# Performance work log

Hardware: AMD Instinct MI355X
Metric: run time of the kernel (lower is better)

Reference implementation:

```python
import jax, jax.numpy as jnp
from jax import lax
import numpy as np

D_MODEL = 1024
N_HEADS = 16
D_STATE = D_MODEL // N_HEADS  # 64
EPS = 1e-6


def setup_inputs() -> dict:
    key = jax.random.key(0)
    ks = jax.random.split(key, 8)
    B, S = 4, 4096
    s = 1.0 / np.sqrt(D_MODEL)
    return {
        "x": jax.random.normal(ks[0], (B, S, D_MODEL), dtype=jnp.float32),
        "state": jnp.zeros((B, N_HEADS, D_STATE), dtype=jnp.float32),
        "norm_w": jnp.ones((D_MODEL,), dtype=jnp.float32),
        "Wp": jax.random.normal(ks[1], (D_MODEL, 3 * N_HEADS * D_STATE), dtype=jnp.float32) * s,
        "bp": jax.random.normal(ks[2], (3 * N_HEADS * D_STATE,), dtype=jnp.float32) * 0.01,
        "Wg": jax.random.normal(ks[3], (D_MODEL, D_MODEL), dtype=jnp.float32) * s,
        "bg": jax.random.normal(ks[4], (D_MODEL,), dtype=jnp.float32) * 0.01,
        "Wo": jax.random.normal(ks[5], (D_MODEL, D_MODEL), dtype=jnp.float32) * s,
        "bo": jax.random.normal(ks[6], (D_MODEL,), dtype=jnp.float32) * 0.01,
    }


def reference(x, state, norm_w, Wp, bp, Wg, bg, Wo, bo):
    B, S, D = x.shape
    # RMSNorm
    rms = jnp.sqrt(jnp.mean(x * x, axis=-1, keepdims=True) + EPS)
    xn = norm_w * x / rms
    # input-dependent gate and SSM parameters (all per-timestep, vectorized)
    gate = jax.nn.sigmoid(xn @ Wg + bg)                        # (B,S,D)
    p = (xn @ Wp + bp).reshape(B, S, N_HEADS, 3, D_STATE)
    delta = jax.nn.sigmoid(p[..., 0, :])                       # (B,S,H,Ds)
    Bt = p[..., 1, :]
    Ct = p[..., 2, :]
    # sequential recurrence h_{t+1} = delta_t * h_t + B_t via lax.scan over time
    def step(h, db):
        d, b = db
        h = d * h + b
        return h, h
    dT = jnp.moveaxis(delta, 1, 0)  # (S,B,H,Ds)
    bT = jnp.moveaxis(Bt, 1, 0)
    new_state, hs = lax.scan(step, state, (dT, bT))
    hs = jnp.moveaxis(hs, 0, 1)     # (B,S,H,Ds)
    ssm = (Ct * hs).reshape(B, S, D)
    mixed = gate * ssm + (1.0 - gate) * xn
    y = mixed @ Wo + bo + x         # out_proj + residual (dropout=0)
    return y, new_state
```

## Files before the change

### kernel.cpp

```cpp
#include <hip/hip_runtime.h>
#include <hip/hip_bf16.h>
#include <cstdint>
#include <cstddef>

#define D_MODEL 1024
#define N_HEADS 16
#define D_STATE 64
#define SEQ 4096
#define BATCH 4
#define M_TOK (BATCH * SEQ)
#define N1 4096
#define CLEN 128
#define NCH (SEQ / CLEN)
#define NCHAN (BATCH * D_MODEL)

typedef __attribute__((ext_vector_type(8))) short bf16x8;
typedef __attribute__((ext_vector_type(4))) float f32x4;

__device__ __forceinline__ float sigmoidf_(float x) {
    return 1.0f / (1.0f + __expf(-x));
}

__device__ __forceinline__ void async_load16(const void* g, void* l) {
    __builtin_amdgcn_global_load_lds(
        (__attribute__((address_space(1))) void*)(g),
        (__attribute__((address_space(3))) void*)(l), 16, 0, 0);
}

__global__ __launch_bounds__(256) void transpose_cvt(
    const float* __restrict__ src, __hip_bfloat16* __restrict__ dst,
    int K, int N)
{
    __shared__ float tile[32][33];
    int n0 = blockIdx.x * 32, k0 = blockIdx.y * 32;
    int tx = threadIdx.x, ty = threadIdx.y;
#pragma unroll
    for (int j = 0; j < 32; j += 8)
        tile[ty + j][tx] = src[(size_t)(k0 + ty + j) * N + n0 + tx];
    __syncthreads();
#pragma unroll
    for (int j = 0; j < 32; j += 8)
        dst[(size_t)(n0 + ty + j) * K + k0 + tx] = __float2bfloat16(tile[tx][ty + j]);
}

__global__ __launch_bounds__(256) void rmsnorm_kernel(
    const float* __restrict__ x, const float* __restrict__ w,
    __hip_bfloat16* __restrict__ xn)
{
    int m = blockIdx.x;
    int tid = threadIdx.x;
    const float4* xr = (const float4*)(x + (size_t)m * D_MODEL);
    float4 v = xr[tid];
    float ss = v.x * v.x + v.y * v.y + v.z * v.z + v.w * v.w;
#pragma unroll
    for (int o = 32; o >= 1; o >>= 1) ss += __shfl_xor(ss, o, 64);
    __shared__ float red[4];
    int wave = tid >> 6, lane = tid & 63;
    if (lane == 0) red[wave] = ss;
    __syncthreads();
    float tot = red[0] + red[1] + red[2] + red[3];
    float scale = rsqrtf(tot * (1.0f / D_MODEL) + 1e-6f);
    const float4* wr = (const float4*)w;
    float4 wv = wr[tid];
    __hip_bfloat16 o4[4];
    o4[0] = __float2bfloat16(wv.x * v.x * scale);
    o4[1] = __float2bfloat16(wv.y * v.y * scale);
    o4[2] = __float2bfloat16(wv.z * v.z * scale);
    o4[3] = __float2bfloat16(wv.w * v.w * scale);
    *(uint64_t*)(xn + (size_t)m * D_MODEL + tid * 4) = *(uint64_t*)o4;
}


template <int MODE>
__global__ __launch_bounds__(512, 2) void gemm256(
    const __hip_bfloat16* __restrict__ A,
    const __hip_bfloat16* __restrict__ Bt,
    const float* __restrict__ bias0,
    const float* __restrict__ bias1,
    void* __restrict__ outp, int N, int K)
{
    extern __shared__ short lds[];
    const int tid = threadIdx.x;
    const int wave = tid >> 6, lane = tid & 63;
    const int fr = lane & 15, fq = lane >> 4;
    const int frx = fr & 7;
    const int wm = (wave >> 2) * 128;
    const int wn = (wave & 3) * 64;

    const int gx = gridDim.x;
    const int nwg = gx * gridDim.y;
    const int orig = blockIdx.y * gx + blockIdx.x;
    const int swz = (orig & 7) * (nwg >> 3) + (orig >> 3);
    const int m0 = (swz / gx) * 256;
    const int n0 = (swz % gx) * 256;

    const int rb = tid >> 3, p8 = tid & 7;
    const int lsl = p8 ^ (rb & 7);
    const short* Ag0 = (const short*)A + (size_t)(m0 + rb) * K + lsl * 8;
    const short* Bg0 = (const short*)Bt + (size_t)(n0 + rb) * K + lsl * 8;
    const int stL = rb * 64 + p8 * 8;

    const int NT = K >> 6;

    f32x4 acc[2][4][4];
#pragma unroll
    for (int h = 0; h < 2; ++h)
#pragma unroll
        for (int i = 0; i < 4; ++i)
#pragma unroll
            for (int j = 0; j < 4; ++j)
                acc[h][i][j] = (f32x4){0.f, 0.f, 0.f, 0.f};

    {
        short* la = lds;
        short* lb = lds + 16384;
        async_load16(Bg0 + (size_t)(0 * 64) * K, lb + stL + 0 * 4096);
        async_load16(Bg0 + (size_t)(1 * 64) * K, lb + stL + 1 * 4096);
        async_load16(Bg0 + (size_t)(2 * 64) * K, lb + stL + 2 * 4096);
        async_load16(Bg0 + (size_t)(3 * 64) * K, lb + stL + 3 * 4096);
        async_load16(Ag0 + (size_t)(0 * 64) * K, la + stL + 0 * 4096);
        async_load16(Ag0 + (size_t)(2 * 64) * K, la + stL + 2 * 4096);
        async_load16(Ag0 + (size_t)(1 * 64) * K, la + stL + 1 * 4096);
        async_load16(Ag0 + (size_t)(3 * 64) * K, la + stL + 3 * 4096);
    }
    asm volatile("s_waitcnt vmcnt(2)" ::: "memory");
    __builtin_amdgcn_s_barrier();
    __builtin_amdgcn_sched_barrier(0);

#define LDA_(base, h, i, kk) (*(const bf16x8*)&(base)[(wm + (h)*64 + (i)*16 + fr) * 64 + \
                                                      (((kk)*4 + fq) ^ frx) * 8])
#define LDB_(base, j, kk)    (*(const bf16x8*)&(base)[(wn + (j)*16 + fr) * 64 + \
                                                      (((kk)*4 + fq) ^ frx) * 8])
#define STAGE_A(c) async_load16(AgN + (size_t)((c) * 64) * K, laN + stL + (c) * 4096)
#define STAGE_B(c) async_load16(BgN + (size_t)((c) * 64) * K, lbN + stL + (c) * 4096)

    bf16x8 afA[4][2], afB[4][2], b0[2][2], b1[2][2];

    {
        const short* Ab = lds;
        const short* Bb = lds + 16384;
#pragma unroll
        for (int i = 0; i < 4; ++i) { afA[i][0] = LDA_(Ab, 0, i, 0); afA[i][1] = LDA_(Ab, 0, i, 1); }
#pragma unroll
        for (int j = 0; j < 2; ++j) { b0[j][0] = LDB_(Bb, j, 0); b0[j][1] = LDB_(Bb, j, 1); }
    }

    for (int t = 0; t < NT; ++t) {
        const short* Ab = lds + ((t & 1) ? 32768 : 0);
        const short* Bb = Ab + 16384;
        short* laN = lds + ((t & 1) ? 0 : 32768);
        short* lbN = laN + 16384;
        const short* AgN = Ag0 + (size_t)(t + 1) * 64;
        const short* BgN = Bg0 + (size_t)(t + 1) * 64;
        const bool pf = (t + 1 < NT);

        if (pf) { STAGE_B(0); STAGE_B(1); }
#pragma unroll
        for (int j = 0; j < 2; ++j) { b1[j][0] = LDB_(Bb, 2 + j, 0); b1[j][1] = LDB_(Bb, 2 + j, 1); }
        __builtin_amdgcn_s_setprio(1);
#pragma unroll
        for (int i = 0; i < 4; ++i)
#pragma unroll
            for (int j = 0; j < 2; ++j) {
                acc[0][i][j] = __builtin_amdgcn_mfma_f32_16x16x32_bf16(afA[i][0], b0[j][0], acc[0][i][j], 0, 0, 0);
                acc[0][i][j] = __builtin_amdgcn_mfma_f32_16x16x32_bf16(afA[i][1], b0[j][1], acc[0][i][j], 0, 0, 0);
            }
        __builtin_amdgcn_s_setprio(0);
        __builtin_amdgcn_sched_barrier(0);

        if (pf) { STAGE_B(2); STAGE_B(3); }
        if (pf) { asm volatile("s_waitcnt vmcnt(4)" ::: "memory"); }
        else    { asm volatile("s_waitcnt vmcnt(0)" ::: "memory"); }
        __builtin_amdgcn_s_barrier();
        __builtin_amdgcn_sched_barrier(0);
#pragma unroll
        for (int i = 0; i < 4; ++i) { afB[i][0] = LDA_(Ab, 1, i, 0); afB[i][1] = LDA_(Ab, 1, i, 1); }
        __builtin_amdgcn_s_setprio(1);
#pragma unroll
        for (int i = 0; i < 4; ++i)
#pragma unroll
            for (int j = 0; j < 2; ++j) {
                acc[0][i][2 + j] = __builtin_amdgcn_mfma_f32_16x16x32_bf16(afA[i][0], b1[j][0], acc[0][i][2 + j], 0, 0, 0);
                acc[0][i][2 + j] = __builtin_amdgcn_mfma_f32_16x16x32_bf16(afA[i][1], b1[j][1], acc[0][i][2 + j], 0, 0, 0);
            }
        __builtin_amdgcn_s_setprio(0);
        __builtin_amdgcn_sched_barrier(0);

        if (pf) { STAGE_A(0); STAGE_A(2); }
        __builtin_amdgcn_s_setprio(1);
#pragma unroll
        for (int i = 0; i < 4; ++i)
#pragma unroll
            for (int j = 0; j < 2; ++j) {
                acc[1][i][j] = __builtin_amdgcn_mfma_f32_16x16x32_bf16(afB[i][0], b0[j][0], acc[1][i][j], 0, 0, 0);
                acc[1][i][j] = __builtin_amdgcn_mfma_f32_16x16x32_bf16(afB[i][1], b0[j][1], acc[1][i][j], 0, 0, 0);
            }
        __builtin_amdgcn_s_setprio(0);
        __builtin_amdgcn_sched_barrier(0);

        if (pf) {
            STAGE_A(1); STAGE_A(3);
            asm volatile("s_waitcnt vmcnt(2)" ::: "memory");
            __builtin_amdgcn_s_barrier();
            __builtin_amdgcn_sched_barrier(0);
            const short* AbN = laN;
            const short* BbN = lbN;
#pragma unroll
            for (int i = 0; i < 4; ++i) { afA[i][0] = LDA_(AbN, 0, i, 0); afA[i][1] = LDA_(AbN, 0, i, 1); }
#pragma unroll
            for (int j = 0; j < 2; ++j) { b0[j][0] = LDB_(BbN, j, 0); b0[j][1] = LDB_(BbN, j, 1); }
        }
        __builtin_amdgcn_s_setprio(1);
#pragma unroll
        for (int i = 0; i < 4; ++i)
#pragma unroll
            for (int j = 0; j < 2; ++j) {
                acc[1][i][2 + j] = __builtin_amdgcn_mfma_f32_16x16x32_bf16(afB[i][0], b1[j][0], acc[1][i][2 + j], 0, 0, 0);
                acc[1][i][2 + j] = __builtin_amdgcn_mfma_f32_16x16x32_bf16(afB[i][1], b1[j][1], acc[1][i][2 + j], 0, 0, 0);
            }
        __builtin_amdgcn_s_setprio(0);
        __builtin_amdgcn_sched_barrier(0);
    }
#undef LDA_
#undef LDB_
#undef STAGE_A
#undef STAGE_B

    if constexpr (MODE == 0) {
        __hip_bfloat16* O = (__hip_bfloat16*)outp;
        float bv[4];
#pragma unroll
        for (int j = 0; j < 4; ++j) {
            int gcol = n0 + wn + j * 16 + fr;
            bv[j] = (gcol < D_MODEL) ? bias0[gcol] : bias1[gcol - D_MODEL];
        }
#pragma unroll
        for (int h = 0; h < 2; ++h)
#pragma unroll
            for (int i = 0; i < 4; ++i)
#pragma unroll
                for (int r = 0; r < 4; ++r) {
                    int grow = m0 + wm + h * 64 + i * 16 + fq * 4 + r;
                    __hip_bfloat16* orow = O + (size_t)grow * N + n0 + wn + fr;
#pragma unroll
                    for (int j = 0; j < 4; ++j)
                        orow[j * 16] = __float2bfloat16(acc[h][i][j][r] + bv[j]);
                }
    } else {
        float* O = (float*)outp;
#pragma unroll
        for (int h = 0; h < 2; ++h)
#pragma unroll
            for (int i = 0; i < 4; ++i)
#pragma unroll
                for (int r = 0; r < 4; ++r) {
                    int grow = m0 + wm + h * 64 + i * 16 + fq * 4 + r;
#pragma unroll
                    for (int j = 0; j < 4; ++j) {
                        int gcol = n0 + wn + j * 16 + fr;
                        O[(size_t)grow * N + gcol] =
                            acc[h][i][j][r] + bias0[gcol] + bias1[(size_t)grow * D_MODEL + gcol];
                    }
                }
    }
}

__global__ __launch_bounds__(256) void scan_part1(
    const __hip_bfloat16* __restrict__ out1,
    float* __restrict__ Abuf, float* __restrict__ Bbuf)
{
    int g = blockIdx.x * 256 + threadIdx.x;
    int chan = g & (NCHAN - 1);
    int c = g >> 12;
    int b = chan >> 10;
    int hd = chan & 1023;
    int h = hd >> 6, d = hd & 63;
    size_t tok0 = (size_t)b * SEQ + (size_t)c * CLEN;
    const __hip_bfloat16* pd = out1 + tok0 * N1 + D_MODEL + h * 192 + d;
    float a = 1.0f, hloc = 0.0f;
#pragma unroll 4
    for (int s = 0; s < CLEN; s++) {
        float dp = __bfloat162float(pd[0]);
        float bt = __bfloat162float(pd[64]);
        float sd = sigmoidf_(dp);
        a *= sd;
        hloc = sd * hloc + bt;
        pd += N1;
    }
    Abuf[c * NCHAN + chan] = a;
    Bbuf[c * NCHAN + chan] = hloc;
}

__global__ __launch_bounds__(256) void scan_comb(
    const float* __restrict__ Abuf, const float* __restrict__ Bbuf,
    const float* __restrict__ state, float* __restrict__ Pbuf,
    float* __restrict__ new_state)
{
    int chan = blockIdx.x * 256 + threadIdx.x;
    float hp = state[chan];
#pragma unroll
    for (int c = 0; c < NCH; c++) {
        Pbuf[c * NCHAN + chan] = hp;
        hp = Abuf[c * NCHAN + chan] * hp + Bbuf[c * NCHAN + chan];
    }
    new_state[chan] = hp;
}

__global__ __launch_bounds__(256) void scan_apply(
    const __hip_bfloat16* __restrict__ out1,
    const __hip_bfloat16* __restrict__ xn,
    const float* __restrict__ Pbuf,
    __hip_bfloat16* __restrict__ mixed)
{
    int g = blockIdx.x * 256 + threadIdx.x;
    int chan = g & (NCHAN - 1);
    int c = g >> 12;
    int b = chan >> 10;
    int hd = chan & 1023;
    int h = hd >> 6, d = hd & 63;
    size_t tok0 = (size_t)b * SEQ + (size_t)c * CLEN;
    const __hip_bfloat16* rbase = out1 + tok0 * N1;
    const __hip_bfloat16* xbase = xn + tok0 * D_MODEL + hd;
    __hip_bfloat16* mbase = mixed + tok0 * D_MODEL + hd;
    const int pcol = D_MODEL + h * 192 + d;
    float hh = Pbuf[c * NCHAN + chan];
#pragma unroll 4
    for (int s = 0; s < CLEN; s++) {
        const __hip_bfloat16* r = rbase + (size_t)s * N1;
        float dp = __bfloat162float(r[pcol]);
        float bt = __bfloat162float(r[pcol + 64]);
        float ct = __bfloat162float(r[pcol + 128]);
        float gp = __bfloat162float(r[hd]);
        float sd = sigmoidf_(dp);
        hh = sd * hh + bt;
        float gg = sigmoidf_(gp);
        float xv = __bfloat162float(xbase[(size_t)s * D_MODEL]);
        mbase[(size_t)s * D_MODEL] = __float2bfloat16(gg * (ct * hh) + (1.0f - gg) * xv);
    }
}

extern "C" void kernel_launch(void* const* d_in, const int* in_sizes, int n_in,
                              void* d_out, int out_size, void* d_ws, size_t ws_size,
                              hipStream_t stream) {
    const float* x      = (const float*)d_in[0];
    const float* state  = (const float*)d_in[1];
    const float* norm_w = (const float*)d_in[2];
    const float* Wp     = (const float*)d_in[3];
    const float* bp     = (const float*)d_in[4];
    const float* Wg     = (const float*)d_in[5];
    const float* bg     = (const float*)d_in[6];
    const float* Wo     = (const float*)d_in[7];
    const float* bo     = (const float*)d_in[8];
    float* out = (float*)d_out;

    __hip_bfloat16* W1T   = (__hip_bfloat16*)d_ws;
    __hip_bfloat16* WoT   = W1T + (size_t)N1 * D_MODEL;
    __hip_bfloat16* xnb   = WoT + (size_t)D_MODEL * D_MODEL;
    __hip_bfloat16* out1  = xnb + (size_t)M_TOK * D_MODEL;
    __hip_bfloat16* mixed = out1 + (size_t)M_TOK * N1;
    float* Abuf = (float*)(mixed + (size_t)M_TOK * D_MODEL);
    float* Bbuf = Abuf + (size_t)NCHAN * NCH;
    float* Pbuf = Bbuf + (size_t)NCHAN * NCH;

    static bool attr_set = false;
    if (!attr_set) {
        hipFuncSetAttribute(reinterpret_cast<const void*>(&gemm256<0>),
                            hipFuncAttributeMaxDynamicSharedMemorySize, 131072);
        hipFuncSetAttribute(reinterpret_cast<const void*>(&gemm256<1>),
                            hipFuncAttributeMaxDynamicSharedMemorySize, 131072);
        attr_set = true;
    }

    dim3 tb(32, 8);
    transpose_cvt<<<dim3(1024 / 32, 1024 / 32), tb, 0, stream>>>(Wg, W1T, 1024, 1024);
    transpose_cvt<<<dim3(3072 / 32, 1024 / 32), tb, 0, stream>>>(
        Wp, W1T + (size_t)D_MODEL * D_MODEL, 1024, 3072);
    transpose_cvt<<<dim3(1024 / 32, 1024 / 32), tb, 0, stream>>>(Wo, WoT, 1024, 1024);

    rmsnorm_kernel<<<M_TOK, 256, 0, stream>>>(x, norm_w, xnb);

    gemm256<0><<<dim3(N1 / 256, M_TOK / 256), 512, 131072, stream>>>(
        xnb, W1T, bg, bp, (void*)out1, N1, D_MODEL);

    scan_part1<<<(NCHAN * NCH) / 256, 256, 0, stream>>>(out1, Abuf, Bbuf);
    scan_comb<<<NCHAN / 256, 256, 0, stream>>>(
        Abuf, Bbuf, state, Pbuf, out + (size_t)M_TOK * D_MODEL);
    scan_apply<<<(NCHAN * NCH) / 256, 256, 0, stream>>>(out1, xnb, Pbuf, mixed);

    gemm256<1><<<dim3(D_MODEL / 256, M_TOK / 256), 512, 131072, stream>>>(
        mixed, WoT, bo, x, (void*)out, D_MODEL, D_MODEL);
}
```

Before: 391.4 us.

## Fuse prep kernels, permute Wp columns, vectorize scans and drop combine kernel

Merges the three weight transposes and RMSNorm into one launch. It permutes Wp columns so delta/B/C become contiguous 1024-wide blocks, and vectorizes the scan kernels to handle four channels per thread with bf16x4 loads. It removes the separate scan_comb kernel by having each chunk recompute its prefix state from the chunk summaries, and halves the chunk length. It also precomputes LDS fragment addresses in the GEMM. These changes cut launch count and uncoalesced scalar loads, at the cost of redundant prefix work that grows with chunk index.

```diff
diff --git a/kernel.cpp b/kernel.cpp
--- a/kernel.cpp
+++ b/kernel.cpp
@@ -10,15 +10,24 @@
 #define BATCH 4
 #define M_TOK (BATCH * SEQ)
 #define N1 4096
-#define CLEN 128
+#define CLEN 64
 #define NCH (SEQ / CLEN)
 #define NCHAN (BATCH * D_MODEL)
 
 typedef __attribute__((ext_vector_type(8))) short bf16x8;
+typedef __attribute__((ext_vector_type(4))) short bf16x4;
 typedef __attribute__((ext_vector_type(4))) float f32x4;
 
 __device__ __forceinline__ float sigmoidf_(float x) {
     return 1.0f / (1.0f + __expf(-x));
+}
+__device__ __forceinline__ float b2f(short s) {
+    union { float f; unsigned u; } v; v.u = ((unsigned)(unsigned short)s) << 16;
+    return v.f;
+}
+__device__ __forceinline__ short f2b(float f) {
+    __hip_bfloat16 h = __float2bfloat16(f);
+    return *(short*)&h;
 }
 
 __device__ __forceinline__ void async_load16(const void* g, void* l) {
@@ -27,49 +36,61 @@
         (__attribute__((address_space(3))) void*)(l), 16, 0, 0);
 }
 
-__global__ __launch_bounds__(256) void transpose_cvt(
-    const float* __restrict__ src, __hip_bfloat16* __restrict__ dst,
-    int K, int N)
+__global__ __launch_bounds__(256) void prep_kernel(
+    const float* __restrict__ Wg, const float* __restrict__ Wp,
+    const float* __restrict__ Wo,
+    const float* __restrict__ x, const float* __restrict__ norm_w,
+    __hip_bfloat16* __restrict__ W1T, __hip_bfloat16* __restrict__ WoT,
+    __hip_bfloat16* __restrict__ xn)
 {
     __shared__ float tile[32][33];
-    int n0 = blockIdx.x * 32, k0 = blockIdx.y * 32;
-    int tx = threadIdx.x, ty = threadIdx.y;
-#pragma unroll
-    for (int j = 0; j < 32; j += 8)
-        tile[ty + j][tx] = src[(size_t)(k0 + ty + j) * N + n0 + tx];
-    __syncthreads();
-#pragma unroll
-    for (int j = 0; j < 32; j += 8)
-        dst[(size_t)(n0 + ty + j) * K + k0 + tx] = __float2bfloat16(tile[tx][ty + j]);
-}
-
-__global__ __launch_bounds__(256) void rmsnorm_kernel(
-    const float* __restrict__ x, const float* __restrict__ w,
-    __hip_bfloat16* __restrict__ xn)
-{
-    int m = blockIdx.x;
-    int tid = threadIdx.x;
-    const float4* xr = (const float4*)(x + (size_t)m * D_MODEL);
-    float4 v = xr[tid];
-    float ss = v.x * v.x + v.y * v.y + v.z * v.z + v.w * v.w;
-#pragma unroll
-    for (int o = 32; o >= 1; o >>= 1) ss += __shfl_xor(ss, o, 64);
     __shared__ float red[4];
-    int wave = tid >> 6, lane = tid & 63;
-    if (lane == 0) red[wave] = ss;
-    __syncthreads();
-    float tot = red[0] + red[1] + red[2] + red[3];
-    float scale = rsqrtf(tot * (1.0f / D_MODEL) + 1e-6f);
-    const float4* wr = (const float4*)w;
-    float4 wv = wr[tid];
-    __hip_bfloat16 o4[4];
-    o4[0] = __float2bfloat16(wv.x * v.x * scale);
-    o4[1] = __float2bfloat16(wv.y * v.y * scale);
-    o4[2] = __float2bfloat16(wv.z * v.z * scale);
-    o4[3] = __float2bfloat16(wv.w * v.w * scale);
-    *(uint64_t*)(xn + (size_t)m * D_MODEL + tid * 4) = *(uint64_t*)o4;
-}
-
+    const int bid = blockIdx.x;
+    const int tid = threadIdx.x;
+
+    if (bid < 5120) {
+        const float* src; __hip_bfloat16* dst; int N, bx, by, perm;
+        if (bid < 1024)      { src = Wg; dst = W1T; N = 1024; bx = bid & 31;          by = bid >> 5;          perm = 0; }
+        else if (bid < 4096) { int l = bid - 1024; src = Wp; dst = W1T; N = 3072; bx = l % 96; by = l / 96;   perm = 1; }
+        else                 { int l = bid - 4096; src = Wo; dst = WoT; N = 1024; bx = l & 31; by = l >> 5;   perm = 0; }
+        int n0 = bx * 32, k0 = by * 32;
+        int tx = tid & 31, ty = tid >> 5;
+#pragma unroll
+        for (int j = 0; j < 32; j += 8)
+            tile[ty + j][tx] = src[(size_t)(k0 + ty + j) * N + n0 + tx];
+        __syncthreads();
+#pragma unroll
+        for (int j = 0; j < 32; j += 8) {
+            int n = n0 + ty + j;
+            int row;
+            if (perm) {
+                int ht = n >> 6;
+                row = 1024 + (ht % 3) * 1024 + (ht / 3) * 64 + (n & 63);
+            } else row = n;
+            dst[(size_t)row * D_MODEL + k0 + tx] = __float2bfloat16(tile[tx][ty + j]);
+        }
+    } else {
+        int m = bid - 5120;
+        const float4* xr = (const float4*)(x + (size_t)m * D_MODEL);
+        float4 v = xr[tid];
+        float ss = v.x * v.x + v.y * v.y + v.z * v.z + v.w * v.w;
+#pragma unroll
+        for (int o = 32; o >= 1; o >>= 1) ss += __shfl_xor(ss, o, 64);
+        int wave = tid >> 6, lane = tid & 63;
+        if (lane == 0) red[wave] = ss;
+        __syncthreads();
+        float tot = red[0] + red[1] + red[2] + red[3];
+        float scale = rsqrtf(tot * (1.0f / D_MODEL) + 1e-6f);
+        const float4* wr = (const float4*)norm_w;
+        float4 wv = wr[tid];
+        __hip_bfloat16 o4[4];
+        o4[0] = __float2bfloat16(wv.x * v.x * scale);
+        o4[1] = __float2bfloat16(wv.y * v.y * scale);
+        o4[2] = __float2bfloat16(wv.z * v.z * scale);
+        o4[3] = __float2bfloat16(wv.w * v.w * scale);
+        *(uint64_t*)(xn + (size_t)m * D_MODEL + tid * 4) = *(uint64_t*)o4;
+    }
+}
 
 template <int MODE>
 __global__ __launch_bounds__(512, 2) void gemm256(
@@ -100,6 +121,11 @@
     const short* Bg0 = (const short*)Bt + (size_t)(n0 + rb) * K + lsl * 8;
     const int stL = rb * 64 + p8 * 8;
 
+    const int laneA = (wm + fr) * 128;
+    const int laneB = (wn + fr) * 128;
+    const int F0 = (fq ^ frx) * 16;
+    const int F1 = ((4 + fq) ^ frx) * 16;
+
     const int NT = K >> 6;
 
     f32x4 acc[2][4][4];
@@ -127,22 +153,21 @@
     __builtin_amdgcn_s_barrier();
     __builtin_amdgcn_sched_barrier(0);
 
-#define LDA_(base, h, i, kk) (*(const bf16x8*)&(base)[(wm + (h)*64 + (i)*16 + fr) * 64 + \
-                                                      (((kk)*4 + fq) ^ frx) * 8])
-#define LDB_(base, j, kk)    (*(const bf16x8*)&(base)[(wn + (j)*16 + fr) * 64 + \
-                                                      (((kk)*4 + fq) ^ frx) * 8])
+#define RD(base, off) (*(const bf16x8*)((base) + (off)))
 #define STAGE_A(c) async_load16(AgN + (size_t)((c) * 64) * K, laN + stL + (c) * 4096)
 #define STAGE_B(c) async_load16(BgN + (size_t)((c) * 64) * K, lbN + stL + (c) * 4096)
 
     bf16x8 afA[4][2], afB[4][2], b0[2][2], b1[2][2];
 
     {
-        const short* Ab = lds;
-        const short* Bb = lds + 16384;
-#pragma unroll
-        for (int i = 0; i < 4; ++i) { afA[i][0] = LDA_(Ab, 0, i, 0); afA[i][1] = LDA_(Ab, 0, i, 1); }
-#pragma unroll
-        for (int j = 0; j < 2; ++j) { b0[j][0] = LDB_(Bb, j, 0); b0[j][1] = LDB_(Bb, j, 1); }
+        const char* bA0 = (const char*)lds + laneA + F0;
+        const char* bA1 = (const char*)lds + laneA + F1;
+        const char* bB0 = (const char*)(lds + 16384) + laneB + F0;
+        const char* bB1 = (const char*)(lds + 16384) + laneB + F1;
+#pragma unroll
+        for (int i = 0; i < 4; ++i) { afA[i][0] = RD(bA0, i * 2048); afA[i][1] = RD(bA1, i * 2048); }
+#pragma unroll
+        for (int j = 0; j < 2; ++j) { b0[j][0] = RD(bB0, j * 2048); b0[j][1] = RD(bB1, j * 2048); }
     }
 
     for (int t = 0; t < NT; ++t) {
@@ -153,10 +178,14 @@
         const short* AgN = Ag0 + (size_t)(t + 1) * 64;
         const short* BgN = Bg0 + (size_t)(t + 1) * 64;
         const bool pf = (t + 1 < NT);
+        const char* bA0 = (const char*)Ab + laneA + F0;
+        const char* bA1 = (const char*)Ab + laneA + F1;
+        const char* bB0 = (const char*)Bb + laneB + F0;
+        const char* bB1 = (const char*)Bb + laneB + F1;
 
         if (pf) { STAGE_B(0); STAGE_B(1); }
 #pragma unroll
-        for (int j = 0; j < 2; ++j) { b1[j][0] = LDB_(Bb, 2 + j, 0); b1[j][1] = LDB_(Bb, 2 + j, 1); }
+        for (int j = 0; j < 2; ++j) { b1[j][0] = RD(bB0, (2 + j) * 2048); b1[j][1] = RD(bB1, (2 + j) * 2048); }
         __builtin_amdgcn_s_setprio(1);
 #pragma unroll
         for (int i = 0; i < 4; ++i)
@@ -174,7 +203,7 @@
         __builtin_amdgcn_s_barrier();
         __builtin_amdgcn_sched_barrier(0);
 #pragma unroll
-        for (int i = 0; i < 4; ++i) { afB[i][0] = LDA_(Ab, 1, i, 0); afB[i][1] = LDA_(Ab, 1, i, 1); }
+        for (int i = 0; i < 4; ++i) { afB[i][0] = RD(bA0, 8192 + i * 2048); afB[i][1] = RD(bA1, 8192 + i * 2048); }
         __builtin_amdgcn_s_setprio(1);
 #pragma unroll
         for (int i = 0; i < 4; ++i)
@@ -203,12 +232,14 @@
             asm volatile("s_waitcnt vmcnt(2)" ::: "memory");
             __builtin_amdgcn_s_barrier();
             __builtin_amdgcn_sched_barrier(0);
-            const short* AbN = laN;
-            const short* BbN = lbN;
-#pragma unroll
-            for (int i = 0; i < 4; ++i) { afA[i][0] = LDA_(AbN, 0, i, 0); afA[i][1] = LDA_(AbN, 0, i, 1); }
-#pragma unroll
-            for (int j = 0; j < 2; ++j) { b0[j][0] = LDB_(BbN, j, 0); b0[j][1] = LDB_(BbN, j, 1); }
+            const char* nA0 = (const char*)laN + laneA + F0;
+            const char* nA1 = (const char*)laN + laneA + F1;
+            const char* nB0 = (const char*)lbN + laneB + F0;
+            const char* nB1 = (const char*)lbN + laneB + F1;
+#pragma unroll
+            for (int i = 0; i < 4; ++i) { afA[i][0] = RD(nA0, i * 2048); afA[i][1] = RD(nA1, i * 2048); }
+#pragma unroll
+            for (int j = 0; j < 2; ++j) { b0[j][0] = RD(nB0, j * 2048); b0[j][1] = RD(nB1, j * 2048); }
         }
         __builtin_amdgcn_s_setprio(1);
 #pragma unroll
@@ -221,8 +252,7 @@
         __builtin_amdgcn_s_setprio(0);
         __builtin_amdgcn_sched_barrier(0);
     }
-#undef LDA_
-#undef LDB_
+#undef RD
 #undef STAGE_A
 #undef STAGE_B
 
@@ -232,7 +262,12 @@
 #pragma unroll
         for (int j = 0; j < 4; ++j) {
             int gcol = n0 + wn + j * 16 + fr;
-            bv[j] = (gcol < D_MODEL) ? bias0[gcol] : bias1[gcol - D_MODEL];
+            if (gcol < D_MODEL) bv[j] = bias0[gcol];
+            else {
+                int q = gcol - D_MODEL;
+                int tt = q >> 10, hd = q & 1023;
+                bv[j] = bias1[(hd >> 6) * 192 + tt * 64 + (hd & 63)];
+            }
         }
 #pragma unroll
         for (int h = 0; h < 2; ++h)
@@ -270,73 +305,77 @@
     float* __restrict__ Abuf, float* __restrict__ Bbuf)
 {
     int g = blockIdx.x * 256 + threadIdx.x;
-    int chan = g & (NCHAN - 1);
-    int c = g >> 12;
-    int b = chan >> 10;
-    int hd = chan & 1023;
-    int h = hd >> 6, d = hd & 63;
+    int cg = g & 1023;
+    int c = g >> 10;
+    int chan0 = cg * 4;
+    int b = chan0 >> 10, hd0 = chan0 & 1023;
     size_t tok0 = (size_t)b * SEQ + (size_t)c * CLEN;
-    const __hip_bfloat16* pd = out1 + tok0 * N1 + D_MODEL + h * 192 + d;
-    float a = 1.0f, hloc = 0.0f;
+    const short* pd = (const short*)out1 + tok0 * N1 + D_MODEL + hd0;
+    float a[4] = {1.f, 1.f, 1.f, 1.f};
+    float hl[4] = {0.f, 0.f, 0.f, 0.f};
 #pragma unroll 4
     for (int s = 0; s < CLEN; s++) {
-        float dp = __bfloat162float(pd[0]);
-        float bt = __bfloat162float(pd[64]);
-        float sd = sigmoidf_(dp);
-        a *= sd;
-        hloc = sd * hloc + bt;
+        bf16x4 dv = *(const bf16x4*)pd;
+        bf16x4 bv = *(const bf16x4*)(pd + 1024);
+#pragma unroll
+        for (int k = 0; k < 4; k++) {
+            float sd = sigmoidf_(b2f(dv[k]));
+            a[k] *= sd;
+            hl[k] = sd * hl[k] + b2f(bv[k]);
+        }
         pd += N1;
     }
-    Abuf[c * NCHAN + chan] = a;
-    Bbuf[c * NCHAN + chan] = hloc;
-}
-
-__global__ __launch_bounds__(256) void scan_comb(
-    const float* __restrict__ Abuf, const float* __restrict__ Bbuf,
-    const float* __restrict__ state, float* __restrict__ Pbuf,
-    float* __restrict__ new_state)
-{
-    int chan = blockIdx.x * 256 + threadIdx.x;
-    float hp = state[chan];
-#pragma unroll
-    for (int c = 0; c < NCH; c++) {
-        Pbuf[c * NCHAN + chan] = hp;
-        hp = Abuf[c * NCHAN + chan] * hp + Bbuf[c * NCHAN + chan];
-    }
-    new_state[chan] = hp;
+    *(f32x4*)&Abuf[c * NCHAN + chan0] = (f32x4){a[0], a[1], a[2], a[3]};
+    *(f32x4*)&Bbuf[c * NCHAN + chan0] = (f32x4){hl[0], hl[1], hl[2], hl[3]};
 }
 
 __global__ __launch_bounds__(256) void scan_apply(
     const __hip_bfloat16* __restrict__ out1,
     const __hip_bfloat16* __restrict__ xn,
-    const float* __restrict__ Pbuf,
-    __hip_bfloat16* __restrict__ mixed)
+    const float* __restrict__ Abuf, const float* __restrict__ Bbuf,
+    const float* __restrict__ state,
+    __hip_bfloat16* __restrict__ mixed, float* __restrict__ new_state)
 {
     int g = blockIdx.x * 256 + threadIdx.x;
-    int chan = g & (NCHAN - 1);
-    int c = g >> 12;
-    int b = chan >> 10;
-    int hd = chan & 1023;
-    int h = hd >> 6, d = hd & 63;
+    int cg = g & 1023;
+    int c = g >> 10;
+    int chan0 = cg * 4;
+    int b = chan0 >> 10, hd0 = chan0 & 1023;
     size_t tok0 = (size_t)b * SEQ + (size_t)c * CLEN;
-    const __hip_bfloat16* rbase = out1 + tok0 * N1;
-    const __hip_bfloat16* xbase = xn + tok0 * D_MODEL + hd;
-    __hip_bfloat16* mbase = mixed + tok0 * D_MODEL + hd;
-    const int pcol = D_MODEL + h * 192 + d;
-    float hh = Pbuf[c * NCHAN + chan];
+
+    f32x4 hp4 = *(const f32x4*)&state[chan0];
+    for (int cc = 0; cc < c; ++cc) {
+        f32x4 av = *(const f32x4*)&Abuf[cc * NCHAN + chan0];
+        f32x4 bv = *(const f32x4*)&Bbuf[cc * NCHAN + chan0];
+        hp4 = av * hp4 + bv;
+    }
+    float hp[4] = {hp4[0], hp4[1], hp4[2], hp4[3]};
+
+    const short* rbase = (const short*)out1 + tok0 * N1;
+    const short* xb = (const short*)xn + tok0 * D_MODEL + hd0;
+    short* mb = (short*)mixed + tok0 * D_MODEL + hd0;
 #pragma unroll 4
     for (int s = 0; s < CLEN; s++) {
-        const __hip_bfloat16* r = rbase + (size_t)s * N1;
-        float dp = __bfloat162float(r[pcol]);
-        float bt = __bfloat162float(r[pcol + 64]);
-        float ct = __bfloat162float(r[pcol + 128]);
-        float gp = __bfloat162float(r[hd]);
-        float sd = sigmoidf_(dp);
-        hh = sd * hh + bt;
-        float gg = sigmoidf_(gp);
-        float xv = __bfloat162float(xbase[(size_t)s * D_MODEL]);
-        mbase[(size_t)s * D_MODEL] = __float2bfloat16(gg * (ct * hh) + (1.0f - gg) * xv);
-    }
+        bf16x4 dv = *(const bf16x4*)(rbase + D_MODEL + hd0);
+        bf16x4 bv = *(const bf16x4*)(rbase + 2048 + hd0);
+        bf16x4 cv = *(const bf16x4*)(rbase + 3072 + hd0);
+        bf16x4 gv = *(const bf16x4*)(rbase + hd0);
+        bf16x4 xv = *(const bf16x4*)xb;
+        bf16x4 ov;
+#pragma unroll
+        for (int k = 0; k < 4; k++) {
+            float sd = sigmoidf_(b2f(dv[k]));
+            hp[k] = sd * hp[k] + b2f(bv[k]);
+            float gg = sigmoidf_(b2f(gv[k]));
+            ov[k] = f2b(gg * (b2f(cv[k]) * hp[k]) + (1.0f - gg) * b2f(xv[k]));
+        }
+        *(bf16x4*)mb = ov;
+        rbase += N1;
+        xb += D_MODEL;
+        mb += D_MODEL;
+    }
+    if (c == NCH - 1)
+        *(f32x4*)&new_state[chan0] = (f32x4){hp[0], hp[1], hp[2], hp[3]};
 }
 
 extern "C" void kernel_launch(void* const* d_in, const int* in_sizes, int n_in,
@@ -360,7 +399,6 @@
     __hip_bfloat16* mixed = out1 + (size_t)M_TOK * N1;
     float* Abuf = (float*)(mixed + (size_t)M_TOK * D_MODEL);
     float* Bbuf = Abuf + (size_t)NCHAN * NCH;
-    float* Pbuf = Bbuf + (size_t)NCHAN * NCH;
 
     static bool attr_set = false;
     if (!attr_set) {
@@ -371,21 +409,16 @@
         attr_set = true;
     }
 
-    dim3 tb(32, 8);
-    transpose_cvt<<<dim3(1024 / 32, 1024 / 32), tb, 0, stream>>>(Wg, W1T, 1024, 1024);
-    transpose_cvt<<<dim3(3072 / 32, 1024 / 32), tb, 0, stream>>>(
-        Wp, W1T + (size_t)D_MODEL * D_MODEL, 1024, 3072);
-    transpose_cvt<<<dim3(1024 / 32, 1024 / 32), tb, 0, stream>>>(Wo, WoT, 1024, 1024);
-
-    rmsnorm_kernel<<<M_TOK, 256, 0, stream>>>(x, norm_w, xnb);
+    prep_kernel<<<5120 + M_TOK, 256, 0, stream>>>(
+        Wg, Wp, Wo, x, norm_w, W1T, WoT, xnb);
 
     gemm256<0><<<dim3(N1 / 256, M_TOK / 256), 512, 131072, stream>>>(
         xnb, W1T, bg, bp, (void*)out1, N1, D_MODEL);
 
-    scan_part1<<<(NCHAN * NCH) / 256, 256, 0, stream>>>(out1, Abuf, Bbuf);
-    scan_comb<<<NCHAN / 256, 256, 0, stream>>>(
-        Abuf, Bbuf, state, Pbuf, out + (size_t)M_TOK * D_MODEL);
-    scan_apply<<<(NCHAN * NCH) / 256, 256, 0, stream>>>(out1, xnb, Pbuf, mixed);
+    scan_part1<<<(NCHAN / 4 * NCH) / 256, 256, 0, stream>>>(out1, Abuf, Bbuf);
+
+    scan_apply<<<(NCHAN / 4 * NCH) / 256, 256, 0, stream>>>(
+        out1, xnb, Abuf, Bbuf, state, mixed, out + (size_t)M_TOK * D_MODEL);
 
     gemm256<1><<<dim3(D_MODEL / 256, M_TOK / 256), 512, 131072, stream>>>(
         mixed, WoT, bo, x, (void*)out, D_MODEL, D_MODEL);
```

After: 392.7 us. About the same (+0.3%).
